# Optimization experiments

Measured on AMD Instinct MI355X. Metric: run time of the kernel, lower is better.

Reference implementation:

```python
import jax, jax.numpy as jnp
import numpy as np

N = 100000      # nodes
E = 1000000     # edges
G = 1024        # graphs
NODE_IN, CLIMBER_IN, HID, OUT, HEADS = 6, 4, 64, 4, 2
SLOPE = 0.2     # PyG GATConv default negative_slope


def gat_conv(x, edge_index, W, att_src, att_dst, bias):
    """PyG GATConv, heads=HEADS, concat=False (mean over heads), add_self_loops=True."""
    heads, ch = att_src.shape
    xp = (x @ W).reshape(-1, heads, ch)                       # [N,H,C]
    a_src = jnp.einsum('nhc,hc->nh', xp, att_src)             # [N,H]
    a_dst = jnp.einsum('nhc,hc->nh', xp, att_dst)
    loops = jnp.arange(x.shape[0])
    src = jnp.concatenate([edge_index[0], loops])             # [E+N]
    dst = jnp.concatenate([edge_index[1], loops])
    e = jax.nn.leaky_relu(a_src[src] + a_dst[dst], SLOPE)     # [E+N,H]
    emax = jax.ops.segment_max(e, dst, num_segments=x.shape[0])
    emax = jnp.where(jnp.isfinite(emax), emax, 0.0)
    ex = jnp.exp(e - emax[dst])
    den = jax.ops.segment_sum(ex, dst, num_segments=x.shape[0])
    alpha = ex / (den[dst] + 1e-16)                           # segment softmax over incoming edges
    msg = xp[src] * alpha[:, :, None]                         # [E+N,H,C]
    agg = jax.ops.segment_sum(msg, dst, num_segments=x.shape[0])  # [N,H,C]
    return agg.mean(axis=1) + bias                            # concat=False -> head mean


def setup_inputs() -> dict:
    key = jax.random.key(0)
    ks = jax.random.split(key, 20)
    s = lambda *d: 1.0 / np.sqrt(d[0])
    inp = {
        'x': jax.random.normal(ks[0], (N, NODE_IN), jnp.float32),
        'edge_index': jax.random.randint(ks[1], (2, E), 0, N),
        'batch': jnp.sort(jax.random.randint(ks[2], (N,), 0, G)),
        'climber': jax.random.normal(ks[3], (G, CLIMBER_IN), jnp.float32),
        # conv1 params
        'W1': jax.random.normal(ks[4], (NODE_IN, HEADS * HID), jnp.float32) * s(NODE_IN),
        'as1': jax.random.normal(ks[5], (HEADS, HID), jnp.float32) * s(HID),
        'ad1': jax.random.normal(ks[6], (HEADS, HID), jnp.float32) * s(HID),
        'b1': jnp.zeros((HID,), jnp.float32),
        # conv2 params
        'W2': jax.random.normal(ks[7], (HID, HEADS * HID), jnp.float32) * s(HID),
        'as2': jax.random.normal(ks[8], (HEADS, HID), jnp.float32) * s(HID),
        'ad2': jax.random.normal(ks[9], (HEADS, HID), jnp.float32) * s(HID),
        'b2': jnp.zeros((HID,), jnp.float32),
        # climber embed
        'Wc': jax.random.normal(ks[10], (CLIMBER_IN, HID), jnp.float32) * s(CLIMBER_IN),
        'bc': jnp.zeros((HID,), jnp.float32),
        # classifier
        'Wm1': jax.random.normal(ks[11], (2 * HID, HID), jnp.float32) * s(2 * HID),
        'bm1': jnp.zeros((HID,), jnp.float32),
        'Wm2': jax.random.normal(ks[12], (HID, OUT), jnp.float32) * s(HID),
        'bm2': jnp.zeros((OUT,), jnp.float32),
    }
    return inp


def reference(x, edge_index, batch, climber, W1, as1, ad1, b1, W2, as2, ad2, b2,
              Wc, bc, Wm1, bm1, Wm2, bm2):
    h = jax.nn.relu(gat_conv(x, edge_index, W1, as1, ad1, b1))
    h = jax.nn.relu(gat_conv(h, edge_index, W2, as2, ad2, b2))
    c = jax.nn.relu(climber @ Wc + bc)            # dropout is identity in eval mode
    z = jnp.concatenate([h, c[batch]], axis=1)    # [N, 2*HID]
    z = jax.nn.relu(z @ Wm1 + bm1)                # dropout identity (eval)
    return z @ Wm2 + bm2                          # [N, OUT]
```

## Files before the change

kernel.cpp:

```cpp
#include <hip/hip_runtime.h>
#include <hip/hip_fp16.h>

#define SLOPE 0.2f

__device__ __forceinline__ float lrelu(float v) { return v >= 0.f ? v : SLOPE * v; }

__device__ __forceinline__ unsigned pack2(float a, float b) {
    __half2 h = __floats2half2_rn(a, b);
    return *reinterpret_cast<unsigned*>(&h);
}
__device__ __forceinline__ float4 h4tof4(uint2 u) {
    __half2 a = *reinterpret_cast<__half2*>(&u.x);
    __half2 b = *reinterpret_cast<__half2*>(&u.y);
    float2 fa = __half22float2(a), fb = __half22float2(b);
    return make_float4(fa.x, fa.y, fb.x, fb.y);
}
__device__ __forceinline__ void acc8(float4& A, float4& B, float a, uint4 u) {
    float4 lo = h4tof4(make_uint2(u.x, u.y));
    float4 hi = h4tof4(make_uint2(u.z, u.w));
    A.x += a * lo.x; A.y += a * lo.y; A.z += a * lo.z; A.w += a * lo.w;
    B.x += a * hi.x; B.y += a * hi.y; B.z += a * hi.z; B.w += a * hi.w;
}

template <int K>
__global__ __launch_bounds__(256)
void k_xp_gemm(const float* __restrict__ x, const float* __restrict__ W,
               const float* __restrict__ as_, const float* __restrict__ ad_,
               __half* __restrict__ xph, float* __restrict__ asrc,
               float* __restrict__ adst, int N) {
    constexpr int ZS = K + 1;
    __shared__ float zs[64 * ZS];
    __shared__ float ws[K * 128];
    const int n0 = blockIdx.x * 64;
    const int t = threadIdx.x;

    for (int i = t; i < K * 32; i += 256) ((float4*)ws)[i] = ((const float4*)W)[i];
    for (int i = t; i < 64 * K; i += 256) {
        int n = i / K, k = i - n * K;
        int gn = n0 + n;
        zs[n * ZS + k] = (gn < N) ? x[(size_t)gn * K + k] : 0.f;
    }
    __syncthreads();

    const int tx = t & 15, ty = t >> 4;
    const int c0a = tx * 4;
    const int c0b = 64 + tx * 4;

    float4 asA = *(const float4*)(as_ + c0a);
    float4 asB = *(const float4*)(as_ + c0b);
    float4 adA = *(const float4*)(ad_ + c0a);
    float4 adB = *(const float4*)(ad_ + c0b);

    float acc[4][8];
    #pragma unroll
    for (int i = 0; i < 4; ++i)
        #pragma unroll
        for (int j = 0; j < 8; ++j) acc[i][j] = 0.f;

    for (int k = 0; k < K; ++k) {
        float4 w0 = *(const float4*)(ws + k * 128 + c0a);
        float4 w1 = *(const float4*)(ws + k * 128 + c0b);
        #pragma unroll
        for (int i = 0; i < 4; ++i) {
            float zv = zs[(ty * 4 + i) * ZS + k];
            acc[i][0] += zv * w0.x; acc[i][1] += zv * w0.y;
            acc[i][2] += zv * w0.z; acc[i][3] += zv * w0.w;
            acc[i][4] += zv * w1.x; acc[i][5] += zv * w1.y;
            acc[i][6] += zv * w1.z; acc[i][7] += zv * w1.w;
        }
    }

    #pragma unroll
    for (int i = 0; i < 4; ++i) {
        int nl = ty * 4 + i, gn = n0 + nl;
        if (gn < N) {
            uint2 ua, ub;
            ua.x = pack2(acc[i][0], acc[i][1]);
            ua.y = pack2(acc[i][2], acc[i][3]);
            ub.x = pack2(acc[i][4], acc[i][5]);
            ub.y = pack2(acc[i][6], acc[i][7]);
            *(uint2*)(xph + (size_t)gn * 128 + c0a) = ua;
            *(uint2*)(xph + (size_t)gn * 128 + c0b) = ub;
        }
        float ps0 = acc[i][0]*asA.x + acc[i][1]*asA.y + acc[i][2]*asA.z + acc[i][3]*asA.w;
        float ps1 = acc[i][4]*asB.x + acc[i][5]*asB.y + acc[i][6]*asB.z + acc[i][7]*asB.w;
        float pd0 = acc[i][0]*adA.x + acc[i][1]*adA.y + acc[i][2]*adA.z + acc[i][3]*adA.w;
        float pd1 = acc[i][4]*adB.x + acc[i][5]*adB.y + acc[i][6]*adB.z + acc[i][7]*adB.w;
        #pragma unroll
        for (int off = 1; off <= 8; off <<= 1) {
            ps0 += __shfl_xor(ps0, off, 64);
            ps1 += __shfl_xor(ps1, off, 64);
            pd0 += __shfl_xor(pd0, off, 64);
            pd1 += __shfl_xor(pd1, off, 64);
        }
        if (tx == 0 && gn < N) {
            asrc[gn * 2]     = ps0;
            asrc[gn * 2 + 1] = ps1;
            adst[gn * 2]     = pd0;
            adst[gn * 2 + 1] = pd1;
        }
    }
}

__global__ void k_hist(const int* __restrict__ dst, int* __restrict__ deg,
                       int* __restrict__ rank, int E) {
    int e = blockIdx.x * blockDim.x + threadIdx.x;
    if (e < E) rank[e] = atomicAdd(&deg[dst[e]], 1);
}

__global__ void k_scan_partial(const int* __restrict__ deg, int* __restrict__ partial, int N) {
    int b = blockIdx.x, t = threadIdx.x;
    int base = b * 1024 + t * 4;
    int s = 0;
    for (int i = 0; i < 4; ++i) { int idx = base + i; if (idx < N) s += deg[idx]; }
    __shared__ int sh[256];
    sh[t] = s; __syncthreads();
    for (int off = 128; off > 0; off >>= 1) { if (t < off) sh[t] += sh[t + off]; __syncthreads(); }
    if (t == 0) partial[b] = sh[0];
}

__global__ void k_scan_final(const int* __restrict__ deg, const int* __restrict__ partial,
                             int* __restrict__ rowptr, int N, int E, int nb) {
    int b = blockIdx.x, t = threadIdx.x;
    __shared__ int shp[256];
    shp[t] = (t < nb) ? partial[t] : 0;
    __syncthreads();
    for (int off = 1; off < 256; off <<= 1) {
        int v = (t >= off) ? shp[t - off] : 0;
        __syncthreads();
        shp[t] += v;
        __syncthreads();
    }
    int pbase = (b > 0) ? shp[b - 1] : 0;
    __syncthreads();

    int base = b * 1024 + t * 4;
    int local[4]; int s = 0;
    for (int i = 0; i < 4; ++i) { int idx = base + i; local[i] = (idx < N) ? deg[idx] : 0; s += local[i]; }
    __shared__ int sh[256];
    int orig = s;
    sh[t] = s; __syncthreads();
    for (int off = 1; off < 256; off <<= 1) {
        int v = (t >= off) ? sh[t - off] : 0;
        __syncthreads();
        sh[t] += v;
        __syncthreads();
    }
    int run = pbase + sh[t] - orig;
    for (int i = 0; i < 4; ++i) {
        int idx = base + i;
        if (idx < N) rowptr[idx] = run;
        run += local[i];
    }
    if (b == 0 && t == 0) rowptr[N] = E;
}

__global__ void k_scatter(const int* __restrict__ src, const int* __restrict__ dst,
                          const int* __restrict__ rowptr, const int* __restrict__ rank,
                          int* __restrict__ csr_src, int E) {
    int e = blockIdx.x * blockDim.x + threadIdx.x;
    if (e >= E) return;
    int d = dst[e];
    csr_src[rowptr[d] + rank[e]] = src[e];
}

__global__ void k_ag(const int* __restrict__ rowptr, const int* __restrict__ csr_src,
                     const float* __restrict__ asrc, const float* __restrict__ adst,
                     const __half* __restrict__ xph, const float* __restrict__ b,
                     float* __restrict__ hout, int N) {
    int tid = blockIdx.x * blockDim.x + threadIdx.x;
    int lane = threadIdx.x & 63;
    int wid = tid >> 6;
    int nw = (gridDim.x * blockDim.x) >> 6;
    const int l  = lane & 31;
    const int hh = lane >> 5;
    const int g8 = (lane >> 3) & 3;
    const int c8 = lane & 7;
    const uint4* xp4 = (const uint4*)xph;
    float4 bb0 = ((const float4*)b)[c8 * 2];
    float4 bb1 = ((const float4*)b)[c8 * 2 + 1];

    for (int n = wid; n < N; n += nw) {
        int rs = rowptr[n], re = rowptr[n + 1], cnt = re - rs;
        float a_dst = adst[n * 2 + hh];
        float eself = __expf(lrelu(asrc[n * 2 + hh] + a_dst));

        float4 accA = make_float4(0.f, 0.f, 0.f, 0.f);
        float4 accB = make_float4(0.f, 0.f, 0.f, 0.f);

        if (cnt <= 32) {
            float ev = 0.f; int s_reg = n;
            if (l < cnt) {
                s_reg = csr_src[rs + l];
                ev = __expf(lrelu(asrc[s_reg * 2 + hh] + a_dst));
            }
            float den = ev + (l == 0 ? eself : 0.f);
            #pragma unroll
            for (int off = 16; off > 0; off >>= 1) den += __shfl_xor(den, off, 64);
            float inv = 1.f / (den + 1e-16f);
            float alpha_l = ev * inv;

            if (g8 == 0) acc8(accA, accB, eself * inv, xp4[(size_t)n * 16 + hh * 8 + c8]);
            int base = (hh << 5) - rs;
            for (int e0 = rs; e0 < re; e0 += 8) {
                int ea = e0 + g8, eb = e0 + 4 + g8;
                bool va = ea < re, vb = eb < re;
                float aa = __shfl(alpha_l, base + ea, 64);
                int   sa = __shfl(s_reg,   base + ea, 64);
                float ab = __shfl(alpha_l, base + eb, 64);
                int   sb = __shfl(s_reg,   base + eb, 64);
                if (!va) { aa = 0.f; sa = n; }
                if (!vb) { ab = 0.f; sb = n; }
                uint4 u1 = xp4[(size_t)sa * 16 + hh * 8 + c8];
                uint4 u2 = xp4[(size_t)sb * 16 + hh * 8 + c8];
                acc8(accA, accB, aa, u1);
                acc8(accA, accB, ab, u2);
            }
        } else {
            float den = (l == 0) ? eself : 0.f;
            for (int e = rs + l; e < re; e += 32)
                den += __expf(lrelu(asrc[csr_src[e] * 2 + hh] + a_dst));
            #pragma unroll
            for (int off = 16; off > 0; off >>= 1) den += __shfl_xor(den, off, 64);
            float inv = 1.f / (den + 1e-16f);
            if (g8 == 0) acc8(accA, accB, eself * inv, xp4[(size_t)n * 16 + hh * 8 + c8]);
            for (int e0 = rs; e0 < re; e0 += 8) {
                int ea = e0 + g8, eb = e0 + 4 + g8;
                bool va = ea < re, vb = eb < re;
                int sa = va ? csr_src[ea] : n;
                int sb = vb ? csr_src[eb] : n;
                float aa = va ? __expf(lrelu(asrc[sa * 2 + hh] + a_dst)) * inv : 0.f;
                float ab = vb ? __expf(lrelu(asrc[sb * 2 + hh] + a_dst)) * inv : 0.f;
                uint4 u1 = xp4[(size_t)sa * 16 + hh * 8 + c8];
                uint4 u2 = xp4[(size_t)sb * 16 + hh * 8 + c8];
                acc8(accA, accB, aa, u1);
                acc8(accA, accB, ab, u2);
            }
        }

        #pragma unroll
        for (int off = 8; off <= 32; off <<= 1) {
            accA.x += __shfl_xor(accA.x, off, 64);
            accA.y += __shfl_xor(accA.y, off, 64);
            accA.z += __shfl_xor(accA.z, off, 64);
            accA.w += __shfl_xor(accA.w, off, 64);
            accB.x += __shfl_xor(accB.x, off, 64);
            accB.y += __shfl_xor(accB.y, off, 64);
            accB.z += __shfl_xor(accB.z, off, 64);
            accB.w += __shfl_xor(accB.w, off, 64);
        }
        if (lane < 8) {
            float4 r0, r1;
            r0.x = fmaxf(accA.x * 0.5f + bb0.x, 0.f);
            r0.y = fmaxf(accA.y * 0.5f + bb0.y, 0.f);
            r0.z = fmaxf(accA.z * 0.5f + bb0.z, 0.f);
            r0.w = fmaxf(accA.w * 0.5f + bb0.w, 0.f);
            r1.x = fmaxf(accB.x * 0.5f + bb1.x, 0.f);
            r1.y = fmaxf(accB.y * 0.5f + bb1.y, 0.f);
            r1.z = fmaxf(accB.z * 0.5f + bb1.z, 0.f);
            r1.w = fmaxf(accB.w * 0.5f + bb1.w, 0.f);
            ((float4*)hout)[(size_t)n * 16 + c8 * 2]     = r0;
            ((float4*)hout)[(size_t)n * 16 + c8 * 2 + 1] = r1;
        }
    }
}

__global__ __launch_bounds__(256)
void k_climber_cpre(const float* __restrict__ climber, const float* __restrict__ Wc,
                    const float* __restrict__ bc, const float* __restrict__ Wm1,
                    const float* __restrict__ bm1, float* __restrict__ cpre, int G) {
    __shared__ float ce[4][64];
    __shared__ float wm1b[64 * 64];
    int t = threadIdx.x;
    for (int i = t; i < 1024; i += 256) ((float4*)wm1b)[i] = ((const float4*)Wm1)[1024 + i];
    int gl = t >> 6, c = t & 63;
    int g = blockIdx.x * 4 + gl;
    float acc = bc[c];
    if (g < G)
        for (int k = 0; k < 4; ++k) acc += climber[g * 4 + k] * Wc[k * 64 + c];
    ce[gl][c] = fmaxf(acc, 0.f);
    __syncthreads();
    float o = bm1[c];
    for (int k = 0; k < 64; ++k) o += ce[gl][k] * wm1b[k * 64 + c];
    if (g < G) cpre[(size_t)g * 64 + c] = o;
}

__global__ __launch_bounds__(256)
void k_final(const float* __restrict__ h2, const float* __restrict__ cpre,
             const int* __restrict__ batch, const float* __restrict__ Wm1,
             const float* __restrict__ Wm2, const float* __restrict__ bm2,
             float* __restrict__ out, int N) {
    __shared__ float zs[64 * 65];
    __shared__ float ws[64 * 64];
    __shared__ float4 w2l[64];
    const int n0 = blockIdx.x * 64;
    const int t = threadIdx.x;

    for (int i = t; i < 1024; i += 256) ((float4*)ws)[i] = ((const float4*)Wm1)[i];
    if (t < 64) w2l[t] = ((const float4*)Wm2)[t];
    for (int i = t; i < 64 * 64; i += 256) {
        int n = i >> 6, k = i & 63;
        int gn = n0 + n;
        zs[n * 65 + k] = (gn < N) ? h2[(size_t)gn * 64 + k] : 0.f;
    }
    __syncthreads();

    const int tx = t & 15, ty = t >> 4;
    const int c0 = tx * 4;
    float acc[4][4];
    #pragma unroll
    for (int i = 0; i < 4; ++i)
        #pragma unroll
        for (int j = 0; j < 4; ++j) acc[i][j] = 0.f;

    for (int k = 0; k < 64; ++k) {
        float4 wv = *(const float4*)(ws + k * 64 + c0);
        #pragma unroll
        for (int i = 0; i < 4; ++i) {
            float zv = zs[(ty * 4 + i) * 65 + k];
            acc[i][0] += zv * wv.x; acc[i][1] += zv * wv.y;
            acc[i][2] += zv * wv.z; acc[i][3] += zv * wv.w;
        }
    }
    __syncthreads();

    float4 wa = w2l[c0], wb = w2l[c0 + 1], wc = w2l[c0 + 2], wd = w2l[c0 + 3];
    #pragma unroll
    for (int i = 0; i < 4; ++i) {
        int nl = ty * 4 + i, gn = n0 + nl;
        float4 o = make_float4(0.f, 0.f, 0.f, 0.f);
        if (gn < N) {
            int b = batch[gn];
            float4 cp = *(const float4*)(cpre + (size_t)b * 64 + c0);
            float m0 = fmaxf(acc[i][0] + cp.x, 0.f);
            float m1 = fmaxf(acc[i][1] + cp.y, 0.f);
            float m2 = fmaxf(acc[i][2] + cp.z, 0.f);
            float m3 = fmaxf(acc[i][3] + cp.w, 0.f);
            o.x = m0 * wa.x + m1 * wb.x + m2 * wc.x + m3 * wd.x;
            o.y = m0 * wa.y + m1 * wb.y + m2 * wc.y + m3 * wd.y;
            o.z = m0 * wa.z + m1 * wb.z + m2 * wc.z + m3 * wd.z;
            o.w = m0 * wa.w + m1 * wb.w + m2 * wc.w + m3 * wd.w;
        }
        *(float4*)(zs + tx * 260 + nl * 4) = o;
    }
    __syncthreads();
    {
        int nl = t >> 2, j = t & 3, gn = n0 + nl;
        float s = 0.f;
        #pragma unroll
        for (int tx2 = 0; tx2 < 16; ++tx2) s += zs[tx2 * 260 + nl * 4 + j];
        if (gn < N) out[(size_t)gn * 4 + j] = s + bm2[j];
    }
}

extern "C" void kernel_launch(void* const* d_in, const int* in_sizes, int n_in,
                              void* d_out, int out_size, void* d_ws, size_t ws_size,
                              hipStream_t stream) {
    const float* x       = (const float*)d_in[0];
    const int*   ei      = (const int*)  d_in[1];
    const int*   batch   = (const int*)  d_in[2];
    const float* climber = (const float*)d_in[3];
    const float* W1  = (const float*)d_in[4];
    const float* as1 = (const float*)d_in[5];
    const float* ad1 = (const float*)d_in[6];
    const float* b1  = (const float*)d_in[7];
    const float* W2  = (const float*)d_in[8];
    const float* as2 = (const float*)d_in[9];
    const float* ad2 = (const float*)d_in[10];
    const float* b2  = (const float*)d_in[11];
    const float* Wc  = (const float*)d_in[12];
    const float* bc  = (const float*)d_in[13];
    const float* Wm1 = (const float*)d_in[14];
    const float* bm1 = (const float*)d_in[15];
    const float* Wm2 = (const float*)d_in[16];
    const float* bm2 = (const float*)d_in[17];

    const int N  = in_sizes[0] / 6;
    const int E  = in_sizes[1] / 2;
    const int G  = in_sizes[3] / 4;

    const int* srcI = ei;
    const int* dstI = ei + E;

    char* base = (char*)d_ws;
    size_t off = 0;
    auto carve = [&](size_t bytes) { void* p = base + off; off += (bytes + 255) & ~size_t(255); return p; };
    __half* xph   = (__half*)carve((size_t)N * 128 * 2);
    float* hbuf   = (float*)carve((size_t)N * 64 * 4);
    float* asrc   = (float*)carve((size_t)N * 2 * 4);
    float* adst   = (float*)carve((size_t)N * 2 * 4);
    float* cpre   = (float*)carve((size_t)G * 64 * 4);
    int*   deg    = (int*)  carve((size_t)N * 4);
    int*   rowptr = (int*)  carve((size_t)(N + 1) * 4);
    int*   rank   = (int*)  carve((size_t)E * 4);
    int*   partial= (int*)  carve(4096 * 4);
    int*   csr_src= (int*)  carve((size_t)E * 4);

    const int tpb = 256;
    const int nScanBlk = (N + 1023) / 1024;
    const int nEdgeBlk = (E + tpb - 1) / tpb;
    const int PG = 2048;
    const int nTile = (N + 63) / 64;

    hipMemsetAsync(deg, 0, (size_t)N * 4, stream);
    k_hist<<<nEdgeBlk, tpb, 0, stream>>>(dstI, deg, rank, E);
    k_scan_partial<<<nScanBlk, tpb, 0, stream>>>(deg, partial, N);
    k_scan_final<<<nScanBlk, tpb, 0, stream>>>(deg, partial, rowptr, N, E, nScanBlk);
    k_scatter<<<nEdgeBlk, tpb, 0, stream>>>(srcI, dstI, rowptr, rank, csr_src, E);

    k_xp_gemm<6><<<nTile, tpb, 0, stream>>>(x, W1, as1, ad1, xph, asrc, adst, N);
    k_ag<<<PG, tpb, 0, stream>>>(rowptr, csr_src, asrc, adst, xph, b1, hbuf, N);

    k_xp_gemm<64><<<nTile, tpb, 0, stream>>>(hbuf, W2, as2, ad2, xph, asrc, adst, N);
    k_ag<<<PG, tpb, 0, stream>>>(rowptr, csr_src, asrc, adst, xph, b2, hbuf, N);

    k_climber_cpre<<<(G + 3) / 4, tpb, 0, stream>>>(climber, Wc, bc, Wm1, bm1, cpre, G);
    k_final<<<nTile, tpb, 0, stream>>>(hbuf, cpre, batch, Wm1, Wm2, bm2, (float*)d_out, N);
}
```

Baseline: 345.4 us.

## Defer softmax normalization, use fma_mix for half accumulation, vectorize tile loads

The aggregation kernel now accumulates unnormalized exp weights and applies 1/den once after the partial reduction. This lets the gather loop start before the denominator reduction finishes. The fp16-to-fp32 convert-and-multiply is replaced with inline v_fma_mix_f32 assembly, and the tail iteration of the short-degree loop is split off. The GEMM and final kernels load their input tiles as float4 instead of scalars. Deferring normalization slightly changes the rounding order, and the inline asm ties the code to the gfx ISA.

```diff
diff --git a/kernel.cpp b/kernel.cpp
--- a/kernel.cpp
+++ b/kernel.cpp
@@ -9,17 +9,19 @@
     __half2 h = __floats2half2_rn(a, b);
     return *reinterpret_cast<unsigned*>(&h);
 }
-__device__ __forceinline__ float4 h4tof4(uint2 u) {
-    __half2 a = *reinterpret_cast<__half2*>(&u.x);
-    __half2 b = *reinterpret_cast<__half2*>(&u.y);
-    float2 fa = __half22float2(a), fb = __half22float2(b);
-    return make_float4(fa.x, fa.y, fb.x, fb.y);
-}
-__device__ __forceinline__ void acc8(float4& A, float4& B, float a, uint4 u) {
-    float4 lo = h4tof4(make_uint2(u.x, u.y));
-    float4 hi = h4tof4(make_uint2(u.z, u.w));
-    A.x += a * lo.x; A.y += a * lo.y; A.z += a * lo.z; A.w += a * lo.w;
-    B.x += a * hi.x; B.y += a * hi.y; B.z += a * hi.z; B.w += a * hi.w;
+
+__device__ __forceinline__ void mix8(float4& A, float4& B, float a, uint4 u) {
+    asm("v_fma_mix_f32 %0, %8, %12, %0 op_sel:[0,0,0] op_sel_hi:[1,0,0]\n\t"
+        "v_fma_mix_f32 %1, %8, %12, %1 op_sel:[1,0,0] op_sel_hi:[1,0,0]\n\t"
+        "v_fma_mix_f32 %2, %9, %12, %2 op_sel:[0,0,0] op_sel_hi:[1,0,0]\n\t"
+        "v_fma_mix_f32 %3, %9, %12, %3 op_sel:[1,0,0] op_sel_hi:[1,0,0]\n\t"
+        "v_fma_mix_f32 %4, %10, %12, %4 op_sel:[0,0,0] op_sel_hi:[1,0,0]\n\t"
+        "v_fma_mix_f32 %5, %10, %12, %5 op_sel:[1,0,0] op_sel_hi:[1,0,0]\n\t"
+        "v_fma_mix_f32 %6, %11, %12, %6 op_sel:[0,0,0] op_sel_hi:[1,0,0]\n\t"
+        "v_fma_mix_f32 %7, %11, %12, %7 op_sel:[1,0,0] op_sel_hi:[1,0,0]"
+        : "+v"(A.x), "+v"(A.y), "+v"(A.z), "+v"(A.w),
+          "+v"(B.x), "+v"(B.y), "+v"(B.z), "+v"(B.w)
+        : "v"(u.x), "v"(u.y), "v"(u.z), "v"(u.w), "v"(a));
 }
 
 template <int K>
@@ -35,10 +37,22 @@
     const int t = threadIdx.x;
 
     for (int i = t; i < K * 32; i += 256) ((float4*)ws)[i] = ((const float4*)W)[i];
-    for (int i = t; i < 64 * K; i += 256) {
-        int n = i / K, k = i - n * K;
-        int gn = n0 + n;
-        zs[n * ZS + k] = (gn < N) ? x[(size_t)gn * K + k] : 0.f;
+    if constexpr (K % 4 == 0) {
+        constexpr int K4 = K / 4;
+        for (int i = t; i < 64 * K4; i += 256) {
+            int n = i / K4, k4 = i - n * K4;
+            int gn = n0 + n;
+            float4 v = (gn < N) ? ((const float4*)x)[(size_t)gn * K4 + k4]
+                                : make_float4(0.f, 0.f, 0.f, 0.f);
+            float* zr = zs + n * ZS + k4 * 4;
+            zr[0] = v.x; zr[1] = v.y; zr[2] = v.z; zr[3] = v.w;
+        }
+    } else {
+        for (int i = t; i < 64 * K; i += 256) {
+            int n = i / K, k = i - n * K;
+            int gn = n0 + n;
+            zs[n * ZS + k] = (gn < N) ? x[(size_t)gn * K + k] : 0.f;
+        }
     }
     __syncthreads();
 
@@ -174,19 +188,22 @@
     int nw = (gridDim.x * blockDim.x) >> 6;
     const int l  = lane & 31;
     const int hh = lane >> 5;
-    const int g8 = (lane >> 3) & 3;
+    const int g4 = (lane >> 3) & 3;
     const int c8 = lane & 7;
+    const int lofs = hh * 8 + c8;
     const uint4* xp4 = (const uint4*)xph;
     float4 bb0 = ((const float4*)b)[c8 * 2];
     float4 bb1 = ((const float4*)b)[c8 * 2 + 1];
 
     for (int n = wid; n < N; n += nw) {
         int rs = rowptr[n], re = rowptr[n + 1], cnt = re - rs;
+        uint4 uself = xp4[(size_t)n * 16 + lofs];
         float a_dst = adst[n * 2 + hh];
         float eself = __expf(lrelu(asrc[n * 2 + hh] + a_dst));
 
         float4 accA = make_float4(0.f, 0.f, 0.f, 0.f);
         float4 accB = make_float4(0.f, 0.f, 0.f, 0.f);
+        float den;
 
         if (cnt <= 32) {
             float ev = 0.f; int s_reg = n;
@@ -194,52 +211,58 @@
                 s_reg = csr_src[rs + l];
                 ev = __expf(lrelu(asrc[s_reg * 2 + hh] + a_dst));
             }
-            float den = ev + (l == 0 ? eself : 0.f);
+            if (g4 == 0) mix8(accA, accB, eself, uself);
+
+            const int base = (hh << 5) - rs;
+            int e0 = rs;
+            for (; e0 + 4 < re; e0 += 8) {
+                int ea = e0 + g4, eb = e0 + 4 + g4;
+                float aa = __shfl(ev,    base + ea, 64);
+                int   sa = __shfl(s_reg, base + ea, 64);
+                float ab = __shfl(ev,    base + eb, 64);
+                int   sb = __shfl(s_reg, base + eb, 64);
+                if (eb >= re) { ab = 0.f; sb = n; }
+                uint4 u1 = xp4[(size_t)sa * 16 + lofs];
+                uint4 u2 = xp4[(size_t)sb * 16 + lofs];
+                mix8(accA, accB, aa, u1);
+                mix8(accA, accB, ab, u2);
+            }
+            if (e0 < re) {
+                int ea = e0 + g4;
+                float aa = __shfl(ev,    base + ea, 64);
+                int   sa = __shfl(s_reg, base + ea, 64);
+                if (ea >= re) { aa = 0.f; sa = n; }
+                uint4 u1 = xp4[(size_t)sa * 16 + lofs];
+                mix8(accA, accB, aa, u1);
+            }
+            den = ev + (l == 0 ? eself : 0.f);
             #pragma unroll
             for (int off = 16; off > 0; off >>= 1) den += __shfl_xor(den, off, 64);
-            float inv = 1.f / (den + 1e-16f);
-            float alpha_l = ev * inv;
-
-            if (g8 == 0) acc8(accA, accB, eself * inv, xp4[(size_t)n * 16 + hh * 8 + c8]);
-            int base = (hh << 5) - rs;
-            for (int e0 = rs; e0 < re; e0 += 8) {
-                int ea = e0 + g8, eb = e0 + 4 + g8;
-                bool va = ea < re, vb = eb < re;
-                float aa = __shfl(alpha_l, base + ea, 64);
-                int   sa = __shfl(s_reg,   base + ea, 64);
-                float ab = __shfl(alpha_l, base + eb, 64);
-                int   sb = __shfl(s_reg,   base + eb, 64);
-                if (!va) { aa = 0.f; sa = n; }
-                if (!vb) { ab = 0.f; sb = n; }
-                uint4 u1 = xp4[(size_t)sa * 16 + hh * 8 + c8];
-                uint4 u2 = xp4[(size_t)sb * 16 + hh * 8 + c8];
-                acc8(accA, accB, aa, u1);
-                acc8(accA, accB, ab, u2);
-            }
         } else {
-            float den = (l == 0) ? eself : 0.f;
+            den = (l == 0) ? eself : 0.f;
             for (int e = rs + l; e < re; e += 32)
                 den += __expf(lrelu(asrc[csr_src[e] * 2 + hh] + a_dst));
             #pragma unroll
             for (int off = 16; off > 0; off >>= 1) den += __shfl_xor(den, off, 64);
-            float inv = 1.f / (den + 1e-16f);
-            if (g8 == 0) acc8(accA, accB, eself * inv, xp4[(size_t)n * 16 + hh * 8 + c8]);
+            if (g4 == 0) mix8(accA, accB, eself, uself);
             for (int e0 = rs; e0 < re; e0 += 8) {
-                int ea = e0 + g8, eb = e0 + 4 + g8;
+                int ea = e0 + g4, eb = e0 + 4 + g4;
                 bool va = ea < re, vb = eb < re;
                 int sa = va ? csr_src[ea] : n;
                 int sb = vb ? csr_src[eb] : n;
-                float aa = va ? __expf(lrelu(asrc[sa * 2 + hh] + a_dst)) * inv : 0.f;
-                float ab = vb ? __expf(lrelu(asrc[sb * 2 + hh] + a_dst)) * inv : 0.f;
-                uint4 u1 = xp4[(size_t)sa * 16 + hh * 8 + c8];
-                uint4 u2 = xp4[(size_t)sb * 16 + hh * 8 + c8];
-                acc8(accA, accB, aa, u1);
-                acc8(accA, accB, ab, u2);
+                float aa = va ? __expf(lrelu(asrc[sa * 2 + hh] + a_dst)) : 0.f;
+                float ab = vb ? __expf(lrelu(asrc[sb * 2 + hh] + a_dst)) : 0.f;
+                uint4 u1 = xp4[(size_t)sa * 16 + lofs];
+                uint4 u2 = xp4[(size_t)sb * 16 + lofs];
+                mix8(accA, accB, aa, u1);
+                mix8(accA, accB, ab, u2);
             }
         }
 
-        #pragma unroll
-        for (int off = 8; off <= 32; off <<= 1) {
+        float inv = 1.f / (den + 1e-16f);
+
+        #pragma unroll
+        for (int off = 8; off <= 16; off <<= 1) {
             accA.x += __shfl_xor(accA.x, off, 64);
             accA.y += __shfl_xor(accA.y, off, 64);
             accA.z += __shfl_xor(accA.z, off, 64);
@@ -249,6 +272,17 @@
             accB.z += __shfl_xor(accB.z, off, 64);
             accB.w += __shfl_xor(accB.w, off, 64);
         }
+        accA.x *= inv; accA.y *= inv; accA.z *= inv; accA.w *= inv;
+        accB.x *= inv; accB.y *= inv; accB.z *= inv; accB.w *= inv;
+        accA.x += __shfl_xor(accA.x, 32, 64);
+        accA.y += __shfl_xor(accA.y, 32, 64);
+        accA.z += __shfl_xor(accA.z, 32, 64);
+        accA.w += __shfl_xor(accA.w, 32, 64);
+        accB.x += __shfl_xor(accB.x, 32, 64);
+        accB.y += __shfl_xor(accB.y, 32, 64);
+        accB.z += __shfl_xor(accB.z, 32, 64);
+        accB.w += __shfl_xor(accB.w, 32, 64);
+
         if (lane < 8) {
             float4 r0, r1;
             r0.x = fmaxf(accA.x * 0.5f + bb0.x, 0.f);
@@ -298,10 +332,13 @@
 
     for (int i = t; i < 1024; i += 256) ((float4*)ws)[i] = ((const float4*)Wm1)[i];
     if (t < 64) w2l[t] = ((const float4*)Wm2)[t];
-    for (int i = t; i < 64 * 64; i += 256) {
-        int n = i >> 6, k = i & 63;
+    for (int i = t; i < 64 * 16; i += 256) {
+        int n = i >> 4, k4 = i & 15;
         int gn = n0 + n;
-        zs[n * 65 + k] = (gn < N) ? h2[(size_t)gn * 64 + k] : 0.f;
+        float4 v = (gn < N) ? ((const float4*)h2)[(size_t)gn * 16 + k4]
+                            : make_float4(0.f, 0.f, 0.f, 0.f);
+        float* zr = zs + n * 65 + k4 * 4;
+        zr[0] = v.x; zr[1] = v.y; zr[2] = v.z; zr[3] = v.w;
     }
     __syncthreads();
 
```

Measured after the change: 330.0 us. 1.05x faster.
